# Kernel tuning notes

Hardware: AMD Instinct MI355X
Metric: run time of the kernel (lower is better)

## Reference

```python
import jax, jax.numpy as jnp
import numpy as np

T, B, F, H, L = 512, 64, 128, 512, 3
SCALES = [1, 2, 4]  # 2**l for l in range(n_layers)


def setup_inputs() -> dict:
    key = jax.random.key(0)
    ks = jax.random.split(key, 10)
    s = 0.05
    inp = {"inputs": jax.random.normal(ks[0], (B, T, F), jnp.float32)}
    in_dims = [F, H, H]
    i = 1
    for l in range(L):
        inp[f"wi{l}"] = jax.random.normal(ks[i], (in_dims[l], H), jnp.float32) * s; i += 1
        inp[f"ws{l}"] = jax.random.normal(ks[i], (F, H), jnp.float32) * s; i += 1
        inp[f"wh{l}"] = jax.random.normal(ks[i], (H, H), jnp.float32) * s; i += 1
    return inp


def _scaled(x, scale):
    # x: [T, B, F]; moving average over time with window `scale`, stride 1
    if scale == 1:
        return x
    cs = jnp.concatenate([jnp.zeros((1,) + x.shape[1:], x.dtype), jnp.cumsum(x, axis=0)], axis=0)
    return (cs[scale:] - cs[:-scale]) / scale  # [T-scale+1, B, F]


def _layer(inp, sx, wi, ws, wh, scale):
    # loop i in range(len(sx) - scale), index = scale-1+i; hidden starts at zeros
    n = sx.shape[0] - scale
    xs = inp[scale - 1:scale - 1 + n]   # [n, B, din]
    sxs = sx[scale - 1:scale - 1 + n]   # [n, B, F]
    h0 = jnp.zeros((inp.shape[1], wh.shape[0]), inp.dtype)

    def step(h, xt):
        x_t, s_t = xt
        h = jnp.tanh(x_t @ wi + h @ wh + s_t @ ws)
        return h, h

    _, out = jax.lax.scan(step, h0, (xs, sxs))
    return out  # [n, B, H]


def reference(inputs, wi0, ws0, wh0, wi1, ws1, wh1, wi2, ws2, wh2):
    x = jnp.transpose(inputs, (1, 0, 2))  # batch_first -> [T, B, F]
    weights = [(wi0, ws0, wh0), (wi1, ws1, wh1), (wi2, ws2, wh2)]
    outs = []
    cur = x
    for l, scale in enumerate(SCALES):
        sx = _scaled(x, scale)  # scaled input always from original sequence
        cur = _layer(cur, sx, *weights[l], scale)
        outs.append(cur)
    return tuple(outs)
```

## Files before the change

kernel.cpp:

```cpp
#include <hip/hip_runtime.h>

#define T_DIM 512
#define B_DIM 64
#define F_DIM 128
#define H_DIM 512

typedef _Float16 f16x8 __attribute__((ext_vector_type(8)));
typedef _Float16 f16x4 __attribute__((ext_vector_type(4)));
typedef float f32x4 __attribute__((ext_vector_type(4)));

__global__ void prep_whT16(_Float16* __restrict__ dst, const float* __restrict__ w0,
                           const float* __restrict__ w1, const float* __restrict__ w2) {
  const long total = 3L * 512 * 512;
  for (long idx = (long)blockIdx.x * blockDim.x + threadIdx.x; idx < total;
       idx += (long)gridDim.x * blockDim.x) {
    int l = (int)(idx >> 18);
    int rem = (int)(idx & 262143);
    int j = rem >> 9, k = rem & 511;
    const float* src = (l == 0) ? w0 : (l == 1) ? w1 : w2;
    dst[idx] = (_Float16)src[k * 512 + j];
  }
}

__global__ void prep_wcat(_Float16* __restrict__ dst,
                          const float* __restrict__ wi0, const float* __restrict__ ws0,
                          const float* __restrict__ wi1, const float* __restrict__ ws1,
                          const float* __restrict__ wi2, const float* __restrict__ ws2) {
  const long total = 3L * 512 * 640;
  for (long idx = (long)blockIdx.x * blockDim.x + threadIdx.x; idx < total;
       idx += (long)gridDim.x * blockDim.x) {
    int l = (int)(idx / 327680);
    int rem = (int)(idx % 327680);
    int n = rem / 640, kc = rem % 640;
    int inK = (l == 0) ? 128 : 512;
    const float* wi = (l == 0) ? wi0 : (l == 1) ? wi1 : wi2;
    const float* ws = (l == 0) ? ws0 : (l == 1) ? ws1 : ws2;
    float v = 0.f;
    if (kc < inK) v = wi[kc * 512 + n];
    else if (kc < inK + 128) v = ws[(kc - inK) * 512 + n];
    dst[idx] = (_Float16)v;
  }
}

__global__ void build_A(_Float16* __restrict__ Abuf, const float* __restrict__ xin,
                        const float* __restrict__ prev, int n, int inK, int scale,
                        int layer) {
  const int Kcat = inK + 128;
  const long total = (long)n * 64 * Kcat;
  for (long idx = (long)blockIdx.x * blockDim.x + threadIdx.x; idx < total;
       idx += (long)gridDim.x * blockDim.x) {
    int k = (int)(idx % Kcat);
    long r = idx / Kcat;
    int b = (int)(r & 63);
    int t = (int)(r >> 6);
    float v;
    if (k < inK) {
      if (layer == 0) v = xin[((long)b * T_DIM + t) * F_DIM + k];
      else v = prev[((long)(t + scale - 1) * B_DIM + b) * H_DIM + k];
    } else {
      int kk = k - inK;
      int t0 = t + scale - 1;
      float s = 0.f;
      for (int w = 0; w < scale; ++w) s += xin[((long)b * T_DIM + t0 + w) * F_DIM + kk];
      v = s * (1.f / scale);
    }
    Abuf[idx] = (_Float16)v;
  }
}

__global__ __launch_bounds__(256) void gemm_f16(const _Float16* __restrict__ A,
                                                const _Float16* __restrict__ Bt,
                                                float* __restrict__ C, int Mrows,
                                                int Kcat) {
  __shared__ _Float16 As[128][72];
  __shared__ _Float16 Bs[128][72];
  const int tid = threadIdx.x;
  const int tn = blockIdx.x, tm = blockIdx.y;
  const int lane = tid & 63, wid = tid >> 6;
  const int wm = wid >> 1, wn = wid & 1;
  f32x4 acc[4][4] = {};
  const int nK = Kcat >> 6;
  const int lrow = tid >> 3, lkc = (tid & 7) * 8;

  for (int kt = 0; kt < nK; ++kt) {
    for (int r = 0; r < 4; ++r) {
      int row = r * 32 + lrow;
      int grow = tm * 128 + row;
      uint4 va = make_uint4(0u, 0u, 0u, 0u);
      if (grow < Mrows) va = *(const uint4*)&A[(size_t)grow * Kcat + kt * 64 + lkc];
      *(uint4*)&As[row][lkc] = va;
      uint4 vb = *(const uint4*)&Bt[(size_t)(tn * 128 + row) * 640 + kt * 64 + lkc];
      *(uint4*)&Bs[row][lkc] = vb;
    }
    __syncthreads();
#pragma unroll
    for (int kk = 0; kk < 64; kk += 32) {
      f16x8 af[4], bf[4];
#pragma unroll
      for (int mt = 0; mt < 4; ++mt)
        af[mt] = *(const f16x8*)&As[wm * 64 + mt * 16 + (lane & 15)][kk + (lane >> 4) * 8];
#pragma unroll
      for (int nt = 0; nt < 4; ++nt)
        bf[nt] = *(const f16x8*)&Bs[wn * 64 + nt * 16 + (lane & 15)][kk + (lane >> 4) * 8];
#pragma unroll
      for (int mt = 0; mt < 4; ++mt)
#pragma unroll
        for (int nt = 0; nt < 4; ++nt)
          acc[mt][nt] = __builtin_amdgcn_mfma_f32_16x16x32_f16(af[mt], bf[nt], acc[mt][nt], 0, 0, 0);
    }
    __syncthreads();
  }

  const int crow0 = tm * 128 + wm * 64 + (lane >> 4) * 4;
  const int ccol0 = tn * 128 + wn * 64 + (lane & 15);
#pragma unroll
  for (int mt = 0; mt < 4; ++mt)
#pragma unroll
    for (int q = 0; q < 4; ++q) {
      int grow = crow0 + mt * 16 + q;
      if (grow < Mrows) {
#pragma unroll
        for (int nt = 0; nt < 4; ++nt)
          C[(size_t)grow * 512 + ccol0 + nt * 16] = acc[mt][nt][q];
      }
    }
}

__global__ __launch_bounds__(512, 2) void rec_fused(float* __restrict__ po,
                                                    const _Float16* __restrict__ whT,
                                                    int n) {
  const int tid = threadIdx.x;
  const int b0g = blockIdx.x * 16;
  const int lane = tid & 63, wid = tid >> 6;
  const int colbase = wid * 64;
  const int bq = lane & 15;
  const int u = lane >> 4;

  __shared__ _Float16 hstage[2][16 * 512];
  __shared__ _Float16 Blds[4 * 32 * 64 * 8];

  {
    uint4* B4 = (uint4*)Blds;
    for (int p = 0; p < 16; ++p) {
      int flat = p * 512 + tid;
      int l = flat & 63;
      int gn = (flat >> 6) & 31;
      int kbl = flat >> 11;
      B4[flat] = *(const uint4*)&whT[(size_t)(gn * 16 + (l & 15)) * 512 +
                                     (kbl + 10) * 32 + (l >> 4) * 8];
    }
  }
  f16x8 bfr[4][10];
  {
#pragma unroll
    for (int nt = 0; nt < 4; ++nt) {
      const int j = colbase + nt * 16 + bq;
#pragma unroll
      for (int kb = 0; kb < 10; ++kb)
        bfr[nt][kb] = *(const f16x8*)&whT[(size_t)j * 512 + kb * 32 + u * 8];
    }
#pragma unroll
    for (int nt = 0; nt < 4; ++nt)
#pragma unroll
      for (int kb = 0; kb < 10; ++kb)
        asm volatile("" : "+v"(bfr[nt][kb]));
  }
  __syncthreads();

  const int gnb = wid * 4;
  const size_t base = (size_t)(b0g + bq) * 512 + colbase + u * 4;

#define AFRD(kb) (*(const f16x8*)&hs[((kb)*64 + u * 16 + (bq ^ (u & 1))) * 8])
#define BLRD(kb, nt) \
  (*(const f16x8*)&Blds[((((kb)-10) * 32 + gnb + (nt)) * 64 + lane) * 8])
#define GLOAD(kb, nt) \
  (*(const f16x8*)&whT[(size_t)(colbase + (nt)*16 + bq) * 512 + (kb)*32 + u * 8])

  for (int t = 0; t < n; ++t) {
    const float* pc = po + (size_t)t * (B_DIM * H_DIM) + base;
    f32x4 pre[4];
#pragma unroll
    for (int nt = 0; nt < 4; ++nt) pre[nt] = *(const f32x4*)&pc[nt * 16];

    f32x4 acc[4] = {};

    if (t > 0) {
      const _Float16* hs = hstage[(t - 1) & 1];
      constexpr int seq[16] = {10, 0, 1, 2, 3, 11, 4, 5, 14, 12, 6, 7, 13, 8, 9, 15};
      constexpr int lnx[16] = {11, -1, -1, -1, -1, 12, -1, -1, -1, 13, -1, -1, -1, -1, -1, -1};
      f16x8 afr[4];
#pragma unroll
      for (int i = 0; i < 4; ++i) afr[i] = AFRD(seq[i]);
      f16x8 blr[4];
#pragma unroll
      for (int nt = 0; nt < 4; ++nt) blr[nt] = BLRD(10, nt);
      f16x8 gfr[4];
#pragma unroll
      for (int nt = 0; nt < 4; ++nt) gfr[nt] = GLOAD(14, nt);

#pragma unroll
      for (int i = 0; i < 16; ++i) {
        const int kb = seq[i];
        f16x8 a = afr[i & 3];
        if (i + 4 < 16) afr[i & 3] = AFRD(seq[i + 4]);
        if (kb < 10) {
#pragma unroll
          for (int nt = 0; nt < 4; ++nt)
            acc[nt] = __builtin_amdgcn_mfma_f32_16x16x32_f16(bfr[nt][kb], a, acc[nt], 0, 0, 0);
        } else if (kb < 14) {
          f16x8 w[4];
#pragma unroll
          for (int nt = 0; nt < 4; ++nt) w[nt] = blr[nt];
          if (lnx[i] >= 0) {
#pragma unroll
            for (int nt = 0; nt < 4; ++nt) blr[nt] = BLRD(lnx[i], nt);
          }
#pragma unroll
          for (int nt = 0; nt < 4; ++nt)
            acc[nt] = __builtin_amdgcn_mfma_f32_16x16x32_f16(w[nt], a, acc[nt], 0, 0, 0);
        } else if (kb == 14) {
          f16x8 w[4];
#pragma unroll
          for (int nt = 0; nt < 4; ++nt) w[nt] = gfr[nt];
#pragma unroll
          for (int nt = 0; nt < 4; ++nt) gfr[nt] = GLOAD(15, nt);
#pragma unroll
          for (int nt = 0; nt < 4; ++nt)
            acc[nt] = __builtin_amdgcn_mfma_f32_16x16x32_f16(w[nt], a, acc[nt], 0, 0, 0);
        } else {
#pragma unroll
          for (int nt = 0; nt < 4; ++nt)
            acc[nt] = __builtin_amdgcn_mfma_f32_16x16x32_f16(gfr[nt], a, acc[nt], 0, 0, 0);
        }
      }
    }

    _Float16* hw = hstage[t & 1];
    float* pw = po + (size_t)t * (B_DIM * H_DIM) + base;
#pragma unroll
    for (int nt = 0; nt < 4; ++nt) {
      const int J = colbase + nt * 16 + u * 4;
      const int slot = (J >> 5) * 64 + ((J >> 3) & 3) * 16 + (bq ^ ((J >> 3) & 1));
      f16x4 h4;
#pragma unroll
      for (int q = 0; q < 4; ++q) {
        float a = acc[nt][q] + pre[nt][q];
        float e = __builtin_amdgcn_exp2f(a * 2.8853900817779268f);
        float h = 1.f - 2.f * __builtin_amdgcn_rcpf(e + 1.f);
        acc[nt][q] = h;
        h4[q] = (_Float16)h;
      }
      *(f16x4*)&hw[slot * 8 + (J & 7)] = h4;
      *(f32x4*)&pw[nt * 16] = acc[nt];
    }
    asm volatile("s_waitcnt lgkmcnt(0)\n\ts_barrier" ::: "memory");
  }
#undef AFRD
#undef BLRD
#undef GLOAD
}

extern "C" void kernel_launch(void* const* d_in, const int* in_sizes, int n_in,
                              void* d_out, int out_size, void* d_ws, size_t ws_size,
                              hipStream_t stream) {
  const float* inputs = (const float*)d_in[0];
  const float* wi[3] = {(const float*)d_in[1], (const float*)d_in[4], (const float*)d_in[7]};
  const float* wsm[3] = {(const float*)d_in[2], (const float*)d_in[5], (const float*)d_in[8]};
  const float* wh[3] = {(const float*)d_in[3], (const float*)d_in[6], (const float*)d_in[9]};
  float* out = (float*)d_out;

  char* wsp = (char*)d_ws;
  _Float16* whT16 = (_Float16*)wsp;
  _Float16* wcat = (_Float16*)(wsp + 1572864);
  _Float16* Abuf = (_Float16*)(wsp + 3538944);

  prep_whT16<<<1024, 256, 0, stream>>>(whT16, wh[0], wh[1], wh[2]);
  prep_wcat<<<1024, 256, 0, stream>>>(wcat, wi[0], wsm[0], wi[1], wsm[1], wi[2], wsm[2]);

  const int nL[3] = {511, 509, 505};
  const long offL[3] = {0L, 511L * 64 * 512, (511L + 509L) * 64 * 512};
  const int inKL[3] = {128, 512, 512};
  const int scaleL[3] = {1, 2, 4};

  for (int l = 0; l < 3; ++l) {
    const int n = nL[l], inK = inKL[l], Kcat = inK + 128;
    const float* prev = (l == 0) ? nullptr : out + offL[l - 1];
    build_A<<<4096, 256, 0, stream>>>(Abuf, inputs, prev, n, inK, scaleL[l], l);
    const int Mrows = n * 64;
    const int Mt = (Mrows + 127) / 128;
    gemm_f16<<<dim3(4, Mt), 256, 0, stream>>>(Abuf, wcat + (size_t)l * 512 * 640,
                                              out + offL[l], Mrows, Kcat);
    rec_fused<<<4, 512, 0, stream>>>(out + offL[l], whT16 + (size_t)l * 262144, n);
  }
}
```

Baseline: 3.538 ms.

## Pipeline all three recurrent layers in one persistent kernel with progress flags

The per-layer build_A/GEMM/recurrence chain is replaced. Only the smoothed-input part of the projection is precomputed by GEMMs up front. A single persistent 28-workgroup kernel then runs the three recurrences at once: dedicated workgroups compute the input projection of the previous layer's hidden states on the fly, synchronised through global atomic progress counters published every 8 steps. This removes the serial layer-by-layer dependency and the large intermediate GEMMs. In exchange it relies on spin-waiting across co-resident workgroups and adds read-modify-write traffic on the output buffer.

```diff
diff --git a/kernel.cpp b/kernel.cpp
--- a/kernel.cpp
+++ b/kernel.cpp
@@ -9,35 +9,31 @@
 typedef _Float16 f16x4 __attribute__((ext_vector_type(4)));
 typedef float f32x4 __attribute__((ext_vector_type(4)));
 
-__global__ void prep_whT16(_Float16* __restrict__ dst, const float* __restrict__ w0,
-                           const float* __restrict__ w1, const float* __restrict__ w2) {
-  const long total = 3L * 512 * 512;
-  for (long idx = (long)blockIdx.x * blockDim.x + threadIdx.x; idx < total;
-       idx += (long)gridDim.x * blockDim.x) {
-    int l = (int)(idx >> 18);
-    int rem = (int)(idx & 262143);
-    int j = rem >> 9, k = rem & 511;
-    const float* src = (l == 0) ? w0 : (l == 1) ? w1 : w2;
+__global__ void prepT(_Float16* __restrict__ dst, const float* __restrict__ src) {
+  int idx = blockIdx.x * blockDim.x + threadIdx.x;
+  if (idx < 262144) {
+    int j = idx >> 9, k = idx & 511;
     dst[idx] = (_Float16)src[k * 512 + j];
   }
 }
 
-__global__ void prep_wcat(_Float16* __restrict__ dst,
-                          const float* __restrict__ wi0, const float* __restrict__ ws0,
-                          const float* __restrict__ wi1, const float* __restrict__ ws1,
-                          const float* __restrict__ wi2, const float* __restrict__ ws2) {
+__global__ void prep_wcat2(_Float16* __restrict__ dst, const float* __restrict__ wi0,
+                           const float* __restrict__ ws0, const float* __restrict__ ws1,
+                           const float* __restrict__ ws2) {
   const long total = 3L * 512 * 640;
   for (long idx = (long)blockIdx.x * blockDim.x + threadIdx.x; idx < total;
        idx += (long)gridDim.x * blockDim.x) {
     int l = (int)(idx / 327680);
     int rem = (int)(idx % 327680);
     int n = rem / 640, kc = rem % 640;
-    int inK = (l == 0) ? 128 : 512;
-    const float* wi = (l == 0) ? wi0 : (l == 1) ? wi1 : wi2;
-    const float* ws = (l == 0) ? ws0 : (l == 1) ? ws1 : ws2;
     float v = 0.f;
-    if (kc < inK) v = wi[kc * 512 + n];
-    else if (kc < inK + 128) v = ws[(kc - inK) * 512 + n];
+    if (l == 0) {
+      if (kc < 128) v = wi0[kc * 512 + n];
+      else if (kc < 256) v = ws0[(kc - 128) * 512 + n];
+    } else {
+      const float* ws = (l == 1) ? ws1 : ws2;
+      if (kc < 128) v = ws[kc * 512 + n];
+    }
     dst[idx] = (_Float16)v;
   }
 }
@@ -126,49 +122,69 @@
     }
 }
 
-__global__ __launch_bounds__(512, 2) void rec_fused(float* __restrict__ po,
-                                                    const _Float16* __restrict__ whT,
-                                                    int n) {
+__global__ void zero_cnt(int* __restrict__ c, int ntot) {
+  int i = blockIdx.x * blockDim.x + threadIdx.x;
+  if (i < ntot) c[i] = 0;
+}
+
+__global__ __launch_bounds__(512, 2) void pipeline(
+    float* __restrict__ out, const _Float16* __restrict__ whT16,
+    const _Float16* __restrict__ wiT16, int* __restrict__ prog) {
+  __shared__ _Float16 stageBuf[2][16 * 512];
+  __shared__ _Float16 Blds[4 * 32 * 64 * 8];
+
+  const int wg = blockIdx.x;
+  const int s = wg >> 2, g = wg & 2 ? (wg & 3) : (wg & 3);
+  const int gg = wg & 3;
+  (void)s; (void)g;
+  const int stage = wg >> 2;
   const int tid = threadIdx.x;
-  const int b0g = blockIdx.x * 16;
   const int lane = tid & 63, wid = tid >> 6;
   const int colbase = wid * 64;
   const int bq = lane & 15;
   const int u = lane >> 4;
-
-  __shared__ _Float16 hstage[2][16 * 512];
-  __shared__ _Float16 Blds[4 * 32 * 64 * 8];
-
-  {
-    uint4* B4 = (uint4*)Blds;
-    for (int p = 0; p < 16; ++p) {
-      int flat = p * 512 + tid;
-      int l = flat & 63;
-      int gn = (flat >> 6) & 31;
-      int kbl = flat >> 11;
-      B4[flat] = *(const uint4*)&whT[(size_t)(gn * 16 + (l & 15)) * 512 +
-                                     (kbl + 10) * 32 + (l >> 4) * 8];
-    }
-  }
-  f16x8 bfr[4][10];
-  {
-#pragma unroll
-    for (int nt = 0; nt < 4; ++nt) {
-      const int j = colbase + nt * 16 + bq;
-#pragma unroll
-      for (int kb = 0; kb < 10; ++kb)
-        bfr[nt][kb] = *(const f16x8*)&whT[(size_t)j * 512 + kb * 32 + u * 8];
-    }
-#pragma unroll
-    for (int nt = 0; nt < 4; ++nt)
-#pragma unroll
-      for (int kb = 0; kb < 10; ++kb)
-        asm volatile("" : "+v"(bfr[nt][kb]));
-  }
-  __syncthreads();
-
   const int gnb = wid * 4;
-  const size_t base = (size_t)(b0g + bq) * 512 + colbase + u * 4;
+
+  const int nL[3] = {511, 509, 505};
+  const size_t offL[3] = {0, 511ul * 32768, (511ul + 509ul) * 32768};
+
+  if ((stage == 0) || (stage == 3) || (stage == 6)) {
+    const int l = stage / 3;
+    const int n = nL[l];
+    float* po = out + offL[l];
+    const _Float16* whT = whT16 + (size_t)l * 262144;
+    int* pub = (l < 2) ? prog + stage * 4 + gg : nullptr;
+    const int* src = (l > 0) ? prog + (stage - 1) * 4 + gg : nullptr;
+    const int b0g = gg * 16;
+
+    {
+      uint4* B4 = (uint4*)Blds;
+      for (int p = 0; p < 16; ++p) {
+        int flat = p * 512 + tid;
+        int ll = flat & 63;
+        int gn = (flat >> 6) & 31;
+        int kbl = flat >> 11;
+        B4[flat] = *(const uint4*)&whT[(size_t)(gn * 16 + (ll & 15)) * 512 +
+                                       (kbl + 10) * 32 + (ll >> 4) * 8];
+      }
+    }
+    f16x8 bfr[4][10];
+    {
+#pragma unroll
+      for (int nt = 0; nt < 4; ++nt) {
+        const int j = colbase + nt * 16 + bq;
+#pragma unroll
+        for (int kb = 0; kb < 10; ++kb)
+          bfr[nt][kb] = *(const f16x8*)&whT[(size_t)j * 512 + kb * 32 + u * 8];
+      }
+#pragma unroll
+      for (int nt = 0; nt < 4; ++nt)
+#pragma unroll
+        for (int kb = 0; kb < 10; ++kb) asm volatile("" : "+v"(bfr[nt][kb]));
+    }
+    __syncthreads();
+
+    const size_t base = (size_t)(b0g + bq) * 512 + colbase + u * 4;
 
 #define AFRD(kb) (*(const f16x8*)&hs[((kb)*64 + u * 16 + (bq ^ (u & 1))) * 8])
 #define BLRD(kb, nt) \
@@ -176,88 +192,239 @@
 #define GLOAD(kb, nt) \
   (*(const f16x8*)&whT[(size_t)(colbase + (nt)*16 + bq) * 512 + (kb)*32 + u * 8])
 
-  for (int t = 0; t < n; ++t) {
-    const float* pc = po + (size_t)t * (B_DIM * H_DIM) + base;
-    f32x4 pre[4];
-#pragma unroll
-    for (int nt = 0; nt < 4; ++nt) pre[nt] = *(const f32x4*)&pc[nt * 16];
-
-    f32x4 acc[4] = {};
-
-    if (t > 0) {
-      const _Float16* hs = hstage[(t - 1) & 1];
-      constexpr int seq[16] = {10, 0, 1, 2, 3, 11, 4, 5, 14, 12, 6, 7, 13, 8, 9, 15};
-      constexpr int lnx[16] = {11, -1, -1, -1, -1, 12, -1, -1, -1, 13, -1, -1, -1, -1, -1, -1};
-      f16x8 afr[4];
-#pragma unroll
-      for (int i = 0; i < 4; ++i) afr[i] = AFRD(seq[i]);
-      f16x8 blr[4];
-#pragma unroll
-      for (int nt = 0; nt < 4; ++nt) blr[nt] = BLRD(10, nt);
-      f16x8 gfr[4];
-#pragma unroll
-      for (int nt = 0; nt < 4; ++nt) gfr[nt] = GLOAD(14, nt);
-
-#pragma unroll
-      for (int i = 0; i < 16; ++i) {
-        const int kb = seq[i];
-        f16x8 a = afr[i & 3];
-        if (i + 4 < 16) afr[i & 3] = AFRD(seq[i + 4]);
-        if (kb < 10) {
-#pragma unroll
-          for (int nt = 0; nt < 4; ++nt)
-            acc[nt] = __builtin_amdgcn_mfma_f32_16x16x32_f16(bfr[nt][kb], a, acc[nt], 0, 0, 0);
-        } else if (kb < 14) {
-          f16x8 w[4];
-#pragma unroll
-          for (int nt = 0; nt < 4; ++nt) w[nt] = blr[nt];
-          if (lnx[i] >= 0) {
-#pragma unroll
-            for (int nt = 0; nt < 4; ++nt) blr[nt] = BLRD(lnx[i], nt);
+    for (int t = 0; t < n; ++t) {
+      if (src && (t & 7) == 0) {
+        if (tid == 0) {
+          int target = t + 8 < n ? t + 8 : n;
+          long it = 0;
+          while (__hip_atomic_load(src, __ATOMIC_ACQUIRE, __HIP_MEMORY_SCOPE_AGENT) < target)
+            if (++it > 100000000L) break;
+        }
+        __syncthreads();
+        __threadfence();
+      }
+
+      const float* pc = po + (size_t)t * 32768 + base;
+      f32x4 pre[4];
+#pragma unroll
+      for (int nt = 0; nt < 4; ++nt) pre[nt] = *(const f32x4*)&pc[nt * 16];
+
+      f32x4 acc[4] = {};
+      if (t > 0) {
+        const _Float16* hs = stageBuf[(t - 1) & 1];
+        constexpr int seq[16] = {10, 0, 1, 2, 3, 11, 4, 5, 14, 12, 6, 7, 13, 8, 9, 15};
+        constexpr int lnx[16] = {11, -1, -1, -1, -1, 12, -1, -1, -1, 13, -1, -1, -1, -1, -1, -1};
+        f16x8 afr[4];
+#pragma unroll
+        for (int i = 0; i < 4; ++i) afr[i] = AFRD(seq[i]);
+        f16x8 blr[4];
+#pragma unroll
+        for (int nt = 0; nt < 4; ++nt) blr[nt] = BLRD(10, nt);
+        f16x8 gfr[4];
+#pragma unroll
+        for (int nt = 0; nt < 4; ++nt) gfr[nt] = GLOAD(14, nt);
+
+#pragma unroll
+        for (int i = 0; i < 16; ++i) {
+          const int kb = seq[i];
+          f16x8 a = afr[i & 3];
+          if (i + 4 < 16) afr[i & 3] = AFRD(seq[i + 4]);
+          if (kb < 10) {
+#pragma unroll
+            for (int nt = 0; nt < 4; ++nt)
+              acc[nt] = __builtin_amdgcn_mfma_f32_16x16x32_f16(bfr[nt][kb], a, acc[nt], 0, 0, 0);
+          } else if (kb < 14) {
+            f16x8 w[4];
+#pragma unroll
+            for (int nt = 0; nt < 4; ++nt) w[nt] = blr[nt];
+            if (lnx[i] >= 0) {
+#pragma unroll
+              for (int nt = 0; nt < 4; ++nt) blr[nt] = BLRD(lnx[i], nt);
+            }
+#pragma unroll
+            for (int nt = 0; nt < 4; ++nt)
+              acc[nt] = __builtin_amdgcn_mfma_f32_16x16x32_f16(w[nt], a, acc[nt], 0, 0, 0);
+          } else if (kb == 14) {
+            f16x8 w[4];
+#pragma unroll
+            for (int nt = 0; nt < 4; ++nt) w[nt] = gfr[nt];
+#pragma unroll
+            for (int nt = 0; nt < 4; ++nt) gfr[nt] = GLOAD(15, nt);
+#pragma unroll
+            for (int nt = 0; nt < 4; ++nt)
+              acc[nt] = __builtin_amdgcn_mfma_f32_16x16x32_f16(w[nt], a, acc[nt], 0, 0, 0);
+          } else {
+#pragma unroll
+            for (int nt = 0; nt < 4; ++nt)
+              acc[nt] = __builtin_amdgcn_mfma_f32_16x16x32_f16(gfr[nt], a, acc[nt], 0, 0, 0);
           }
-#pragma unroll
-          for (int nt = 0; nt < 4; ++nt)
-            acc[nt] = __builtin_amdgcn_mfma_f32_16x16x32_f16(w[nt], a, acc[nt], 0, 0, 0);
-        } else if (kb == 14) {
-          f16x8 w[4];
-#pragma unroll
-          for (int nt = 0; nt < 4; ++nt) w[nt] = gfr[nt];
-#pragma unroll
-          for (int nt = 0; nt < 4; ++nt) gfr[nt] = GLOAD(15, nt);
-#pragma unroll
-          for (int nt = 0; nt < 4; ++nt)
-            acc[nt] = __builtin_amdgcn_mfma_f32_16x16x32_f16(w[nt], a, acc[nt], 0, 0, 0);
-        } else {
-#pragma unroll
-          for (int nt = 0; nt < 4; ++nt)
-            acc[nt] = __builtin_amdgcn_mfma_f32_16x16x32_f16(gfr[nt], a, acc[nt], 0, 0, 0);
         }
       }
-    }
-
-    _Float16* hw = hstage[t & 1];
-    float* pw = po + (size_t)t * (B_DIM * H_DIM) + base;
-#pragma unroll
-    for (int nt = 0; nt < 4; ++nt) {
-      const int J = colbase + nt * 16 + u * 4;
-      const int slot = (J >> 5) * 64 + ((J >> 3) & 3) * 16 + (bq ^ ((J >> 3) & 1));
-      f16x4 h4;
-#pragma unroll
-      for (int q = 0; q < 4; ++q) {
-        float a = acc[nt][q] + pre[nt][q];
-        float e = __builtin_amdgcn_exp2f(a * 2.8853900817779268f);
-        float h = 1.f - 2.f * __builtin_amdgcn_rcpf(e + 1.f);
-        acc[nt][q] = h;
-        h4[q] = (_Float16)h;
-      }
-      *(f16x4*)&hw[slot * 8 + (J & 7)] = h4;
-      *(f32x4*)&pw[nt * 16] = acc[nt];
-    }
-    asm volatile("s_waitcnt lgkmcnt(0)\n\ts_barrier" ::: "memory");
-  }
+
+      _Float16* hw = stageBuf[t & 1];
+      float* pw = po + (size_t)t * 32768 + base;
+#pragma unroll
+      for (int nt = 0; nt < 4; ++nt) {
+        const int J = colbase + nt * 16 + u * 4;
+        const int slot = (J >> 5) * 64 + ((J >> 3) & 3) * 16 + (bq ^ ((J >> 3) & 1));
+        f16x4 h4;
+#pragma unroll
+        for (int q = 0; q < 4; ++q) {
+          float a = acc[nt][q] + pre[nt][q];
+          float e = __builtin_amdgcn_exp2f(a * 2.8853900817779268f);
+          float h = 1.f - 2.f * __builtin_amdgcn_rcpf(e + 1.f);
+          acc[nt][q] = h;
+          h4[q] = (_Float16)h;
+        }
+        *(f16x4*)&hw[slot * 8 + (J & 7)] = h4;
+        *(f32x4*)&pw[nt * 16] = acc[nt];
+      }
+
+      if (pub && (((t & 7) == 7) || (t == n - 1))) {
+        asm volatile("s_waitcnt vmcnt(0) lgkmcnt(0)\n\ts_barrier" ::: "memory");
+        __threadfence();
+        if (tid == 0)
+          __hip_atomic_store(pub, t + 1, __ATOMIC_RELEASE, __HIP_MEMORY_SCOPE_AGENT);
+      } else {
+        asm volatile("s_waitcnt lgkmcnt(0)\n\ts_barrier" ::: "memory");
+      }
+    }
 #undef AFRD
 #undef BLRD
 #undef GLOAD
+  } else {
+    const int l = (stage <= 2) ? 1 : 2;
+    const int ha = (stage == 2 || stage == 5) ? 1 : 0;
+    const int n = nL[l], nprev = nL[l - 1];
+    const int off = (l == 1) ? 1 : 3;
+    const float* xsrc = out + offL[l - 1];
+    float* pdst = out + offL[l];
+    const _Float16* wiT = wiT16 + (size_t)(l - 1) * 262144;
+    int* pub = prog + stage * 4 + gg;
+    const int* srcX = prog + ((l == 1) ? 0 : 3) * 4 + gg;
+    const int* srcA = ha ? (prog + (stage - 1) * 4 + gg) : nullptr;
+
+    f16x8 bfr8[4][8];
+    {
+#pragma unroll
+      for (int nt = 0; nt < 4; ++nt) {
+        const int j = colbase + nt * 16 + bq;
+#pragma unroll
+        for (int kb = 0; kb < 8; ++kb)
+          bfr8[nt][kb] = *(const f16x8*)&wiT[(size_t)j * 512 + (ha * 8 + kb) * 32 + u * 8];
+      }
+#pragma unroll
+      for (int nt = 0; nt < 4; ++nt)
+#pragma unroll
+        for (int kb = 0; kb < 8; ++kb) asm volatile("" : "+v"(bfr8[nt][kb]));
+    }
+
+    const int bx = tid & 15;
+    const int jbi = tid >> 4;
+    const int slotW = (jbi >> 2) * 64 + (jbi & 3) * 16 + (bx ^ (jbi & 1));
+    const size_t xrowbase = (size_t)(gg * 16 + bx) * 512 + ha * 256 + jbi * 8;
+    const size_t base = (size_t)(gg * 16 + bq) * 512 + colbase + u * 4;
+
+    if (tid == 0) {
+      int target = 9 + off < nprev ? 9 + off : nprev;
+      long it = 0;
+      while (__hip_atomic_load(srcX, __ATOMIC_ACQUIRE, __HIP_MEMORY_SCOPE_AGENT) < target)
+        if (++it > 100000000L) break;
+      if (srcA) {
+        int ta = 8 < n ? 8 : n;
+        it = 0;
+        while (__hip_atomic_load(srcA, __ATOMIC_ACQUIRE, __HIP_MEMORY_SCOPE_AGENT) < ta)
+          if (++it > 100000000L) break;
+      }
+    }
+    __syncthreads();
+    __threadfence();
+    {
+      const float* xr = xsrc + (size_t)off * 32768 + xrowbase;
+      float4 xa = *(const float4*)&xr[0];
+      float4 xb = *(const float4*)&xr[4];
+      f16x8 xh;
+      xh[0] = (_Float16)xa.x; xh[1] = (_Float16)xa.y;
+      xh[2] = (_Float16)xa.z; xh[3] = (_Float16)xa.w;
+      xh[4] = (_Float16)xb.x; xh[5] = (_Float16)xb.y;
+      xh[6] = (_Float16)xb.z; xh[7] = (_Float16)xb.w;
+      *(f16x8*)&stageBuf[0][slotW * 8] = xh;
+    }
+    asm volatile("s_waitcnt lgkmcnt(0)\n\ts_barrier" ::: "memory");
+
+#define AFP(kb) \
+  (*(const f16x8*)&hs[((kb)*64 + u * 16 + (bq ^ (u & 1))) * 8])
+
+    for (int t = 0; t < n; ++t) {
+      if ((t & 7) == 0 && t) {
+        if (tid == 0) {
+          int target = t + 9 + off < nprev ? t + 9 + off : nprev;
+          long it = 0;
+          while (__hip_atomic_load(srcX, __ATOMIC_ACQUIRE, __HIP_MEMORY_SCOPE_AGENT) < target)
+            if (++it > 100000000L) break;
+          if (srcA) {
+            int ta = t + 8 < n ? t + 8 : n;
+            it = 0;
+            while (__hip_atomic_load(srcA, __ATOMIC_ACQUIRE, __HIP_MEMORY_SCOPE_AGENT) < ta)
+              if (++it > 100000000L) break;
+          }
+        }
+        __syncthreads();
+        __threadfence();
+      }
+
+      const bool havN = (t + 1 < n);
+      float4 xa, xb;
+      if (havN) {
+        const float* xr = xsrc + (size_t)(t + 1 + off) * 32768 + xrowbase;
+        xa = *(const float4*)&xr[0];
+        xb = *(const float4*)&xr[4];
+      }
+
+      f32x4 acc[4] = {};
+      {
+        const _Float16* hs = stageBuf[t & 1];
+        f16x8 afr[4];
+#pragma unroll
+        for (int i = 0; i < 4; ++i) afr[i] = AFP(i);
+#pragma unroll
+        for (int kb = 0; kb < 8; ++kb) {
+          f16x8 a = afr[kb & 3];
+          if (kb < 4) afr[kb & 3] = AFP(kb + 4);
+#pragma unroll
+          for (int nt = 0; nt < 4; ++nt)
+            acc[nt] = __builtin_amdgcn_mfma_f32_16x16x32_f16(bfr8[nt][kb], a, acc[nt], 0, 0, 0);
+        }
+      }
+
+      float* pw = pdst + (size_t)t * 32768 + base;
+#pragma unroll
+      for (int nt = 0; nt < 4; ++nt) {
+        f32x4 v = *(const f32x4*)&pw[nt * 16];
+        v += acc[nt];
+        *(f32x4*)&pw[nt * 16] = v;
+      }
+
+      if (havN) {
+        f16x8 xh;
+        xh[0] = (_Float16)xa.x; xh[1] = (_Float16)xa.y;
+        xh[2] = (_Float16)xa.z; xh[3] = (_Float16)xa.w;
+        xh[4] = (_Float16)xb.x; xh[5] = (_Float16)xb.y;
+        xh[6] = (_Float16)xb.z; xh[7] = (_Float16)xb.w;
+        *(f16x8*)&stageBuf[(t + 1) & 1][slotW * 8] = xh;
+      }
+
+      if (((t & 7) == 7) || (t == n - 1)) {
+        asm volatile("s_waitcnt vmcnt(0) lgkmcnt(0)\n\ts_barrier" ::: "memory");
+        __threadfence();
+        if (tid == 0)
+          __hip_atomic_store(pub, t + 1, __ATOMIC_RELEASE, __HIP_MEMORY_SCOPE_AGENT);
+      } else {
+        asm volatile("s_waitcnt lgkmcnt(0)\n\ts_barrier" ::: "memory");
+      }
+    }
+#undef AFP
+  }
 }
 
 extern "C" void kernel_launch(void* const* d_in, const int* in_sizes, int n_in,
@@ -271,25 +438,30 @@
 
   char* wsp = (char*)d_ws;
   _Float16* whT16 = (_Float16*)wsp;
-  _Float16* wcat = (_Float16*)(wsp + 1572864);
-  _Float16* Abuf = (_Float16*)(wsp + 3538944);
-
-  prep_whT16<<<1024, 256, 0, stream>>>(whT16, wh[0], wh[1], wh[2]);
-  prep_wcat<<<1024, 256, 0, stream>>>(wcat, wi[0], wsm[0], wi[1], wsm[1], wi[2], wsm[2]);
+  _Float16* wiT16 = (_Float16*)(wsp + 1572864);
+  _Float16* wcat = (_Float16*)(wsp + 2621440);
+  int* prog = (int*)(wsp + 4587520);
+  _Float16* Abuf = (_Float16*)(wsp + 4587776);
+
+  zero_cnt<<<1, 64, 0, stream>>>(prog, 24);
+  for (int l = 0; l < 3; ++l)
+    prepT<<<1024, 256, 0, stream>>>(whT16 + (size_t)l * 262144, wh[l]);
+  prepT<<<1024, 256, 0, stream>>>(wiT16, wi[1]);
+  prepT<<<1024, 256, 0, stream>>>(wiT16 + 262144, wi[2]);
+  prep_wcat2<<<1024, 256, 0, stream>>>(wcat, wi[0], wsm[0], wsm[1], wsm[2]);
 
   const int nL[3] = {511, 509, 505};
-  const long offL[3] = {0L, 511L * 64 * 512, (511L + 509L) * 64 * 512};
-  const int inKL[3] = {128, 512, 512};
-  const int scaleL[3] = {1, 2, 4};
-
-  for (int l = 0; l < 3; ++l) {
-    const int n = nL[l], inK = inKL[l], Kcat = inK + 128;
-    const float* prev = (l == 0) ? nullptr : out + offL[l - 1];
-    build_A<<<4096, 256, 0, stream>>>(Abuf, inputs, prev, n, inK, scaleL[l], l);
-    const int Mrows = n * 64;
-    const int Mt = (Mrows + 127) / 128;
-    gemm_f16<<<dim3(4, Mt), 256, 0, stream>>>(Abuf, wcat + (size_t)l * 512 * 640,
-                                              out + offL[l], Mrows, Kcat);
-    rec_fused<<<4, 512, 0, stream>>>(out + offL[l], whT16 + (size_t)l * 262144, n);
-  }
-}
+  const long offL[3] = {0L, 511L * 32768, (511L + 509L) * 32768};
+
+  build_A<<<4096, 256, 0, stream>>>(Abuf, inputs, nullptr, nL[0], 128, 1, 0);
+  gemm_f16<<<dim3(4, (nL[0] * 64 + 127) / 128), 256, 0, stream>>>(
+      Abuf, wcat, out, nL[0] * 64, 256);
+  build_A<<<2048, 256, 0, stream>>>(Abuf, inputs, nullptr, nL[1], 0, 2, 1);
+  gemm_f16<<<dim3(4, (nL[1] * 64 + 127) / 128), 256, 0, stream>>>(
+      Abuf, wcat + 512 * 640, out + offL[1], nL[1] * 64, 128);
+  build_A<<<2048, 256, 0, stream>>>(Abuf, inputs, nullptr, nL[2], 0, 4, 1);
+  gemm_f16<<<dim3(4, (nL[2] * 64 + 127) / 128), 256, 0, stream>>>(
+      Abuf, wcat + 2 * 512 * 640, out + offL[2], nL[2] * 64, 128);
+
+  pipeline<<<28, 512, 0, stream>>>(out, whT16, wiT16, prog);
+}
```

After: 2.964 ms. 1.19x faster.

## Pipeline the three recurrent layers in time chunks with interleaved input GEMMs

Applied to the files above, without the earlier changes.

Splits the layers' input GEMMs so the scaled-input parts are precomputed up front, while each previous-layer hidden projection runs as a chunked GEMM. A single kernel per wavefront step runs the recurrence for all three layers on different 32-step time chunks concurrently, alongside the GEMM blocks that add the prior layer's chunk contribution. This replaces three serial 4-block recurrences with a wavefront schedule that overlaps them across layers. In exchange it adds about 22 launches that each restage weights and reload the carried hidden state from global memory in fp16.

```diff
diff --git a/kernel.cpp b/kernel.cpp
--- a/kernel.cpp
+++ b/kernel.cpp
@@ -4,40 +4,38 @@
 #define B_DIM 64
 #define F_DIM 128
 #define H_DIM 512
+#define CHS 32
+#define NCH 16
 
 typedef _Float16 f16x8 __attribute__((ext_vector_type(8)));
 typedef _Float16 f16x4 __attribute__((ext_vector_type(4)));
 typedef float f32x4 __attribute__((ext_vector_type(4)));
 
-__global__ void prep_whT16(_Float16* __restrict__ dst, const float* __restrict__ w0,
-                           const float* __restrict__ w1, const float* __restrict__ w2) {
-  const long total = 3L * 512 * 512;
-  for (long idx = (long)blockIdx.x * blockDim.x + threadIdx.x; idx < total;
-       idx += (long)gridDim.x * blockDim.x) {
-    int l = (int)(idx >> 18);
-    int rem = (int)(idx & 262143);
-    int j = rem >> 9, k = rem & 511;
-    const float* src = (l == 0) ? w0 : (l == 1) ? w1 : w2;
+__global__ void prepT(_Float16* __restrict__ dst, const float* __restrict__ src) {
+  int idx = blockIdx.x * blockDim.x + threadIdx.x;
+  if (idx < 262144) {
+    int j = idx >> 9, k = idx & 511;
     dst[idx] = (_Float16)src[k * 512 + j];
   }
 }
 
-__global__ void prep_wcat(_Float16* __restrict__ dst,
-                          const float* __restrict__ wi0, const float* __restrict__ ws0,
-                          const float* __restrict__ wi1, const float* __restrict__ ws1,
-                          const float* __restrict__ wi2, const float* __restrict__ ws2) {
+__global__ void prep_wcat2(_Float16* __restrict__ dst, const float* __restrict__ wi0,
+                           const float* __restrict__ ws0, const float* __restrict__ ws1,
+                           const float* __restrict__ ws2) {
   const long total = 3L * 512 * 640;
   for (long idx = (long)blockIdx.x * blockDim.x + threadIdx.x; idx < total;
        idx += (long)gridDim.x * blockDim.x) {
     int l = (int)(idx / 327680);
     int rem = (int)(idx % 327680);
     int n = rem / 640, kc = rem % 640;
-    int inK = (l == 0) ? 128 : 512;
-    const float* wi = (l == 0) ? wi0 : (l == 1) ? wi1 : wi2;
-    const float* ws = (l == 0) ? ws0 : (l == 1) ? ws1 : ws2;
     float v = 0.f;
-    if (kc < inK) v = wi[kc * 512 + n];
-    else if (kc < inK + 128) v = ws[(kc - inK) * 512 + n];
+    if (l == 0) {
+      if (kc < 128) v = wi0[kc * 512 + n];
+      else if (kc < 256) v = ws0[(kc - 128) * 512 + n];
+    } else {
+      const float* ws = (l == 1) ? ws1 : ws2;
+      if (kc < 128) v = ws[kc * 512 + n];
+    }
     dst[idx] = (_Float16)v;
   }
 }
@@ -126,49 +124,83 @@
     }
 }
 
-__global__ __launch_bounds__(512, 2) void rec_fused(float* __restrict__ po,
-                                                    const _Float16* __restrict__ whT,
-                                                    int n) {
+__global__ __launch_bounds__(512, 2) void pipe_step(
+    float* __restrict__ out0, float* __restrict__ out1, float* __restrict__ out2,
+    const _Float16* __restrict__ whT16, const _Float16* __restrict__ wiT16,
+    int ca, int cb, int cc, int cd, int ce) {
+  __shared__ char ldsRaw[163840];
+  const int blk = blockIdx.x;
   const int tid = threadIdx.x;
-  const int b0g = blockIdx.x * 16;
   const int lane = tid & 63, wid = tid >> 6;
-  const int colbase = wid * 64;
-  const int bq = lane & 15;
-  const int u = lane >> 4;
-
-  __shared__ _Float16 hstage[2][16 * 512];
-  __shared__ _Float16 Blds[4 * 32 * 64 * 8];
-
-  {
-    uint4* B4 = (uint4*)Blds;
-    for (int p = 0; p < 16; ++p) {
-      int flat = p * 512 + tid;
-      int l = flat & 63;
-      int gn = (flat >> 6) & 31;
-      int kbl = flat >> 11;
-      B4[flat] = *(const uint4*)&whT[(size_t)(gn * 16 + (l & 15)) * 512 +
-                                     (kbl + 10) * 32 + (l >> 4) * 8];
-    }
-  }
-  f16x8 bfr[4][10];
-  {
-#pragma unroll
-    for (int nt = 0; nt < 4; ++nt) {
-      const int j = colbase + nt * 16 + bq;
-#pragma unroll
-      for (int kb = 0; kb < 10; ++kb)
-        bfr[nt][kb] = *(const f16x8*)&whT[(size_t)j * 512 + kb * 32 + u * 8];
-    }
-#pragma unroll
-    for (int nt = 0; nt < 4; ++nt)
-#pragma unroll
-      for (int kb = 0; kb < 10; ++kb)
-        asm volatile("" : "+v"(bfr[nt][kb]));
-  }
-  __syncthreads();
-
-  const int gnb = wid * 4;
-  const size_t base = (size_t)(b0g + bq) * 512 + colbase + u * 4;
+  const int nL[3] = {511, 509, 505};
+
+  if (blk < 12) {
+    const int l = blk >> 2;
+    const int gg = blk & 3;
+    const int chunk = (l == 0) ? ca : (l == 1) ? cb : cc;
+    if (chunk < 0 || chunk >= NCH) return;
+    const int n = nL[l];
+    const int s0 = chunk * CHS;
+    if (s0 >= n) return;
+    const int ns = (s0 + CHS < n) ? CHS : (n - s0);
+    float* po = (l == 0) ? out0 : (l == 1) ? out1 : out2;
+    const _Float16* whT = whT16 + (size_t)l * 262144;
+
+    _Float16* hstage = (_Float16*)ldsRaw;
+    _Float16* Blds = (_Float16*)(ldsRaw + 32768);
+
+    const int colbase = wid * 64;
+    const int bq = lane & 15;
+    const int u = lane >> 4;
+    const int gnb = wid * 4;
+
+    {
+      uint4* B4 = (uint4*)Blds;
+      for (int p = 0; p < 16; ++p) {
+        int flat = p * 512 + tid;
+        int ll = flat & 63;
+        int gn = (flat >> 6) & 31;
+        int kbl = flat >> 11;
+        B4[flat] = *(const uint4*)&whT[(size_t)(gn * 16 + (ll & 15)) * 512 +
+                                       (kbl + 10) * 32 + (ll >> 4) * 8];
+      }
+    }
+    f16x8 bfr[4][10];
+    {
+#pragma unroll
+      for (int nt = 0; nt < 4; ++nt) {
+        const int j = colbase + nt * 16 + bq;
+#pragma unroll
+        for (int kb = 0; kb < 10; ++kb)
+          bfr[nt][kb] = *(const f16x8*)&whT[(size_t)j * 512 + kb * 32 + u * 8];
+      }
+#pragma unroll
+      for (int nt = 0; nt < 4; ++nt)
+#pragma unroll
+        for (int kb = 0; kb < 10; ++kb) asm volatile("" : "+v"(bfr[nt][kb]));
+    }
+    if (s0 > 0) {
+      _Float16* hw0 = hstage + ((s0 - 1) & 1) * 8192;
+      for (int rep = 0; rep < 2; ++rep) {
+        int idx = rep * 512 + tid;
+        int lb = idx >> 6;
+        int j0 = (idx & 63) * 8;
+        const float* s = po + (size_t)(s0 - 1) * 32768 + (size_t)(gg * 16 + lb) * 512 + j0;
+        float4 x0 = *(const float4*)s;
+        float4 x1 = *(const float4*)(s + 4);
+        f16x8 hv;
+        hv[0] = (_Float16)x0.x; hv[1] = (_Float16)x0.y;
+        hv[2] = (_Float16)x0.z; hv[3] = (_Float16)x0.w;
+        hv[4] = (_Float16)x1.x; hv[5] = (_Float16)x1.y;
+        hv[6] = (_Float16)x1.z; hv[7] = (_Float16)x1.w;
+        int slot = (j0 >> 5) * 64 + ((j0 >> 3) & 3) * 16 + (lb ^ ((j0 >> 3) & 1));
+        *(f16x8*)&hw0[slot * 8] = hv;
+      }
+    }
+    __syncthreads();
+
+    const int b0g = gg * 16;
+    const size_t base = (size_t)(b0g + bq) * 512 + colbase + u * 4;
 
 #define AFRD(kb) (*(const f16x8*)&hs[((kb)*64 + u * 16 + (bq ^ (u & 1))) * 8])
 #define BLRD(kb, nt) \
@@ -176,88 +208,171 @@
 #define GLOAD(kb, nt) \
   (*(const f16x8*)&whT[(size_t)(colbase + (nt)*16 + bq) * 512 + (kb)*32 + u * 8])
 
-  for (int t = 0; t < n; ++t) {
-    const float* pc = po + (size_t)t * (B_DIM * H_DIM) + base;
-    f32x4 pre[4];
-#pragma unroll
-    for (int nt = 0; nt < 4; ++nt) pre[nt] = *(const f32x4*)&pc[nt * 16];
-
-    f32x4 acc[4] = {};
-
-    if (t > 0) {
-      const _Float16* hs = hstage[(t - 1) & 1];
-      constexpr int seq[16] = {10, 0, 1, 2, 3, 11, 4, 5, 14, 12, 6, 7, 13, 8, 9, 15};
-      constexpr int lnx[16] = {11, -1, -1, -1, -1, 12, -1, -1, -1, 13, -1, -1, -1, -1, -1, -1};
-      f16x8 afr[4];
-#pragma unroll
-      for (int i = 0; i < 4; ++i) afr[i] = AFRD(seq[i]);
-      f16x8 blr[4];
-#pragma unroll
-      for (int nt = 0; nt < 4; ++nt) blr[nt] = BLRD(10, nt);
-      f16x8 gfr[4];
-#pragma unroll
-      for (int nt = 0; nt < 4; ++nt) gfr[nt] = GLOAD(14, nt);
-
-#pragma unroll
-      for (int i = 0; i < 16; ++i) {
-        const int kb = seq[i];
-        f16x8 a = afr[i & 3];
-        if (i + 4 < 16) afr[i & 3] = AFRD(seq[i + 4]);
-        if (kb < 10) {
-#pragma unroll
-          for (int nt = 0; nt < 4; ++nt)
-            acc[nt] = __builtin_amdgcn_mfma_f32_16x16x32_f16(bfr[nt][kb], a, acc[nt], 0, 0, 0);
-        } else if (kb < 14) {
-          f16x8 w[4];
-#pragma unroll
-          for (int nt = 0; nt < 4; ++nt) w[nt] = blr[nt];
-          if (lnx[i] >= 0) {
-#pragma unroll
-            for (int nt = 0; nt < 4; ++nt) blr[nt] = BLRD(lnx[i], nt);
+    for (int t = s0; t < s0 + ns; ++t) {
+      const float* pc = po + (size_t)t * 32768 + base;
+      f32x4 pre[4];
+#pragma unroll
+      for (int nt = 0; nt < 4; ++nt) pre[nt] = *(const f32x4*)&pc[nt * 16];
+
+      f32x4 acc[4] = {};
+      if (t > 0) {
+        const _Float16* hs = hstage + ((t - 1) & 1) * 8192;
+        constexpr int seq[16] = {10, 0, 1, 2, 3, 11, 4, 5, 14, 12, 6, 7, 13, 8, 9, 15};
+        constexpr int lnx[16] = {11, -1, -1, -1, -1, 12, -1, -1, -1, 13, -1, -1, -1, -1, -1, -1};
+        f16x8 afr[4];
+#pragma unroll
+        for (int i = 0; i < 4; ++i) afr[i] = AFRD(seq[i]);
+        f16x8 blr[4];
+#pragma unroll
+        for (int nt = 0; nt < 4; ++nt) blr[nt] = BLRD(10, nt);
+        f16x8 gfr[4];
+#pragma unroll
+        for (int nt = 0; nt < 4; ++nt) gfr[nt] = GLOAD(14, nt);
+
+#pragma unroll
+        for (int i = 0; i < 16; ++i) {
+          const int kb = seq[i];
+          f16x8 a = afr[i & 3];
+          if (i + 4 < 16) afr[i & 3] = AFRD(seq[i + 4]);
+          if (kb < 10) {
+#pragma unroll
+            for (int nt = 0; nt < 4; ++nt)
+              acc[nt] = __builtin_amdgcn_mfma_f32_16x16x32_f16(bfr[nt][kb], a, acc[nt], 0, 0, 0);
+          } else if (kb < 14) {
+            f16x8 w[4];
+#pragma unroll
+            for (int nt = 0; nt < 4; ++nt) w[nt] = blr[nt];
+            if (lnx[i] >= 0) {
+#pragma unroll
+              for (int nt = 0; nt < 4; ++nt) blr[nt] = BLRD(lnx[i], nt);
+            }
+#pragma unroll
+            for (int nt = 0; nt < 4; ++nt)
+              acc[nt] = __builtin_amdgcn_mfma_f32_16x16x32_f16(w[nt], a, acc[nt], 0, 0, 0);
+          } else if (kb == 14) {
+            f16x8 w[4];
+#pragma unroll
+            for (int nt = 0; nt < 4; ++nt) w[nt] = gfr[nt];
+#pragma unroll
+            for (int nt = 0; nt < 4; ++nt) gfr[nt] = GLOAD(15, nt);
+#pragma unroll
+            for (int nt = 0; nt < 4; ++nt)
+              acc[nt] = __builtin_amdgcn_mfma_f32_16x16x32_f16(w[nt], a, acc[nt], 0, 0, 0);
+          } else {
+#pragma unroll
+            for (int nt = 0; nt < 4; ++nt)
+              acc[nt] = __builtin_amdgcn_mfma_f32_16x16x32_f16(gfr[nt], a, acc[nt], 0, 0, 0);
           }
-#pragma unroll
-          for (int nt = 0; nt < 4; ++nt)
-            acc[nt] = __builtin_amdgcn_mfma_f32_16x16x32_f16(w[nt], a, acc[nt], 0, 0, 0);
-        } else if (kb == 14) {
-          f16x8 w[4];
-#pragma unroll
-          for (int nt = 0; nt < 4; ++nt) w[nt] = gfr[nt];
-#pragma unroll
-          for (int nt = 0; nt < 4; ++nt) gfr[nt] = GLOAD(15, nt);
-#pragma unroll
-          for (int nt = 0; nt < 4; ++nt)
-            acc[nt] = __builtin_amdgcn_mfma_f32_16x16x32_f16(w[nt], a, acc[nt], 0, 0, 0);
-        } else {
-#pragma unroll
-          for (int nt = 0; nt < 4; ++nt)
-            acc[nt] = __builtin_amdgcn_mfma_f32_16x16x32_f16(gfr[nt], a, acc[nt], 0, 0, 0);
         }
       }
-    }
-
-    _Float16* hw = hstage[t & 1];
-    float* pw = po + (size_t)t * (B_DIM * H_DIM) + base;
-#pragma unroll
-    for (int nt = 0; nt < 4; ++nt) {
-      const int J = colbase + nt * 16 + u * 4;
-      const int slot = (J >> 5) * 64 + ((J >> 3) & 3) * 16 + (bq ^ ((J >> 3) & 1));
-      f16x4 h4;
-#pragma unroll
-      for (int q = 0; q < 4; ++q) {
-        float a = acc[nt][q] + pre[nt][q];
-        float e = __builtin_amdgcn_exp2f(a * 2.8853900817779268f);
-        float h = 1.f - 2.f * __builtin_amdgcn_rcpf(e + 1.f);
-        acc[nt][q] = h;
-        h4[q] = (_Float16)h;
-      }
-      *(f16x4*)&hw[slot * 8 + (J & 7)] = h4;
-      *(f32x4*)&pw[nt * 16] = acc[nt];
-    }
-    asm volatile("s_waitcnt lgkmcnt(0)\n\ts_barrier" ::: "memory");
-  }
+
+      _Float16* hw = hstage + (t & 1) * 8192;
+      float* pw = po + (size_t)t * 32768 + base;
+#pragma unroll
+      for (int nt = 0; nt < 4; ++nt) {
+        const int J = colbase + nt * 16 + u * 4;
+        const int slot = (J >> 5) * 64 + ((J >> 3) & 3) * 16 + (bq ^ ((J >> 3) & 1));
+        f16x4 h4;
+#pragma unroll
+        for (int q = 0; q < 4; ++q) {
+          float a = acc[nt][q] + pre[nt][q];
+          float e = __builtin_amdgcn_exp2f(a * 2.8853900817779268f);
+          float h = 1.f - 2.f * __builtin_amdgcn_rcpf(e + 1.f);
+          acc[nt][q] = h;
+          h4[q] = (_Float16)h;
+        }
+        *(f16x4*)&hw[slot * 8 + (J & 7)] = h4;
+        *(f32x4*)&pw[nt * 16] = acc[nt];
+      }
+      asm volatile("s_waitcnt lgkmcnt(0)\n\ts_barrier" ::: "memory");
+    }
 #undef AFRD
 #undef BLRD
 #undef GLOAD
+  } else {
+    const int gi = blk - 12;
+    const int which = gi >> 5;
+    const int g = gi & 31;
+    const int chunk = which ? ce : cd;
+    if (chunk < 0 || chunk >= NCH) return;
+    const int l = which + 1;
+    const int n = nL[l];
+    const int t0 = chunk * CHS;
+    if (t0 >= n) return;
+    const int t1 = (t0 + CHS < n) ? (t0 + CHS) : n;
+    const int Mrows = (t1 - t0) * 64;
+    const int Mbase = t0 * 64;
+    const int toff = which ? 3 : 1;
+    const float* hsrc = which ? out1 : out0;
+    float* C = which ? out2 : out1;
+    const _Float16* Bt = wiT16 + (size_t)which * 262144;
+
+    const int tm = g >> 1, tn = g & 1;
+    _Float16(*As)[72] = (_Float16(*)[72])ldsRaw;
+    _Float16(*Bs)[72] = (_Float16(*)[72])(ldsRaw + 128 * 72 * 2);
+    const int wm = wid >> 2, wn = wid & 3;
+    f32x4 acc[4][4] = {};
+
+    for (int kt = 0; kt < 8; ++kt) {
+      for (int rep = 0; rep < 2; ++rep) {
+        int idx = rep * 512 + tid;
+        int row = idx >> 3;
+        int kc8 = (idx & 7) * 8;
+        f16x8 hv = {};
+        if (tm * 128 + row < Mrows) {
+          int grow = Mbase + tm * 128 + row;
+          int tt = grow >> 6, bb = grow & 63;
+          const float* s = hsrc + (size_t)(tt + toff) * 32768 + (size_t)bb * 512 + kt * 64 + kc8;
+          float4 x0 = *(const float4*)s;
+          float4 x1 = *(const float4*)(s + 4);
+          hv[0] = (_Float16)x0.x; hv[1] = (_Float16)x0.y;
+          hv[2] = (_Float16)x0.z; hv[3] = (_Float16)x0.w;
+          hv[4] = (_Float16)x1.x; hv[5] = (_Float16)x1.y;
+          hv[6] = (_Float16)x1.z; hv[7] = (_Float16)x1.w;
+        }
+        *(f16x8*)&As[row][kc8] = hv;
+      }
+      for (int rep = 0; rep < 4; ++rep) {
+        int idx = rep * 512 + tid;
+        int row = idx >> 3;
+        int kc8 = (idx & 7) * 8;
+        *(uint4*)&Bs[row][kc8] =
+            *(const uint4*)&Bt[(size_t)(tn * 256 + row) * 512 + kt * 64 + kc8];
+      }
+      __syncthreads();
+#pragma unroll
+      for (int kk = 0; kk < 64; kk += 32) {
+        f16x8 af[4], bf[4];
+#pragma unroll
+        for (int mt = 0; mt < 4; ++mt)
+          af[mt] = *(const f16x8*)&As[wm * 64 + mt * 16 + (lane & 15)][kk + (lane >> 4) * 8];
+#pragma unroll
+        for (int nt = 0; nt < 4; ++nt)
+          bf[nt] = *(const f16x8*)&Bs[wn * 64 + nt * 16 + (lane & 15)][kk + (lane >> 4) * 8];
+#pragma unroll
+        for (int mt = 0; mt < 4; ++mt)
+#pragma unroll
+          for (int nt = 0; nt < 4; ++nt)
+            acc[mt][nt] = __builtin_amdgcn_mfma_f32_16x16x32_f16(af[mt], bf[nt], acc[mt][nt], 0, 0, 0);
+      }
+      __syncthreads();
+    }
+
+    const int crow0 = tm * 128 + wm * 64 + (lane >> 4) * 4;
+    const int ccol0 = tn * 256 + wn * 64 + (lane & 15);
+#pragma unroll
+    for (int mt = 0; mt < 4; ++mt)
+#pragma unroll
+      for (int q = 0; q < 4; ++q) {
+        int lrow = crow0 + mt * 16 + q;
+        if (lrow < Mrows) {
+          size_t grow = (size_t)(Mbase + lrow);
+#pragma unroll
+          for (int nt = 0; nt < 4; ++nt)
+            C[grow * 512 + ccol0 + nt * 16] += acc[mt][nt][q];
+        }
+      }
+  }
 }
 
 extern "C" void kernel_launch(void* const* d_in, const int* in_sizes, int n_in,
@@ -271,25 +386,33 @@
 
   char* wsp = (char*)d_ws;
   _Float16* whT16 = (_Float16*)wsp;
-  _Float16* wcat = (_Float16*)(wsp + 1572864);
-  _Float16* Abuf = (_Float16*)(wsp + 3538944);
-
-  prep_whT16<<<1024, 256, 0, stream>>>(whT16, wh[0], wh[1], wh[2]);
-  prep_wcat<<<1024, 256, 0, stream>>>(wcat, wi[0], wsm[0], wi[1], wsm[1], wi[2], wsm[2]);
+  _Float16* wiT16 = (_Float16*)(wsp + 1572864);
+  _Float16* wcat = (_Float16*)(wsp + 2621440);
+  _Float16* Abuf = (_Float16*)(wsp + 4587520);
+
+  for (int l = 0; l < 3; ++l)
+    prepT<<<1024, 256, 0, stream>>>(whT16 + (size_t)l * 262144, wh[l]);
+  prepT<<<1024, 256, 0, stream>>>(wiT16, wi[1]);
+  prepT<<<1024, 256, 0, stream>>>(wiT16 + 262144, wi[2]);
+  prep_wcat2<<<1024, 256, 0, stream>>>(wcat, wi[0], wsm[0], wsm[1], wsm[2]);
 
   const int nL[3] = {511, 509, 505};
-  const long offL[3] = {0L, 511L * 64 * 512, (511L + 509L) * 64 * 512};
-  const int inKL[3] = {128, 512, 512};
-  const int scaleL[3] = {1, 2, 4};
-
-  for (int l = 0; l < 3; ++l) {
-    const int n = nL[l], inK = inKL[l], Kcat = inK + 128;
-    const float* prev = (l == 0) ? nullptr : out + offL[l - 1];
-    build_A<<<4096, 256, 0, stream>>>(Abuf, inputs, prev, n, inK, scaleL[l], l);
-    const int Mrows = n * 64;
-    const int Mt = (Mrows + 127) / 128;
-    gemm_f16<<<dim3(4, Mt), 256, 0, stream>>>(Abuf, wcat + (size_t)l * 512 * 640,
-                                              out + offL[l], Mrows, Kcat);
-    rec_fused<<<4, 512, 0, stream>>>(out + offL[l], whT16 + (size_t)l * 262144, n);
-  }
-}
+  const long offL[3] = {0L, 511L * 32768, (511L + 509L) * 32768};
+  float* out0 = out;
+  float* out1 = out + offL[1];
+  float* out2 = out + offL[2];
+
+  build_A<<<4096, 256, 0, stream>>>(Abuf, inputs, nullptr, nL[0], 128, 1, 0);
+  gemm_f16<<<dim3(4, (nL[0] * 64 + 127) / 128), 256, 0, stream>>>(
+      Abuf, wcat, out0, nL[0] * 64, 256);
+  build_A<<<2048, 256, 0, stream>>>(Abuf, inputs, nullptr, nL[1], 0, 2, 1);
+  gemm_f16<<<dim3(4, (nL[1] * 64 + 127) / 128), 256, 0, stream>>>(
+      Abuf, wcat + 512 * 640, out1, nL[1] * 64, 128);
+  build_A<<<2048, 256, 0, stream>>>(Abuf, inputs, nullptr, nL[2], 0, 4, 1);
+  gemm_f16<<<dim3(4, (nL[2] * 64 + 127) / 128), 256, 0, stream>>>(
+      Abuf, wcat + 2 * 512 * 640, out2, nL[2] * 64, 128);
+
+  for (int i = 0; i <= NCH + 5; ++i)
+    pipe_step<<<76, 512, 0, stream>>>(out0, out1, out2, whT16, wiT16,
+                                      i, i - 3, i - 6, i - 2, i - 5);
+}
```

After: 2.916 ms, median of 2. 17.6% less time.
